# Kernel optimization log

Hardware: AMD Instinct MI355X
Metric: run time of the kernel (lower is better)

Reference implementation:

```python
import jax, jax.numpy as jnp
import numpy as np

B, D, F, T = 8192, 128, 128, 64


def setup_inputs() -> dict:
    key = jax.random.key(0)
    k1, k2, k3, k4 = jax.random.split(key, 4)
    inputs = jax.random.normal(k1, (B, D), dtype=jnp.float32)
    task_idx = jax.random.randint(k2, (B,), 0, T, dtype=jnp.int32)
    # default_kernel_init: normal * 1/sqrt(shape[1]) where shape=(T, D, F)
    kernels = jax.random.normal(k3, (T, D, F), dtype=jnp.float32) / jnp.sqrt(float(D))
    biases = jnp.zeros((T, F), dtype=jnp.float32)
    return {"inputs": inputs, "task_idx": task_idx, "kernels": kernels, "biases": biases}


def reference(inputs, task_idx, kernels, biases):
    # MoEDense forward (vector task_idx branch):
    #   y[b] = inputs[b] @ kernels[task_idx[b]] + biases[task_idx[b]]
    t = jnp.clip(task_idx, 0, kernels.shape[0] - 1)
    k_g = jnp.take(kernels, t, axis=0)          # [B, D, F] per-sample expert gather
    y = jnp.einsum('bd,bdf->bf', inputs, k_g)   # per-sample vec-mat
    y = y + jnp.take(biases, t, axis=0)
    return y
```

## Files before the change

### kernel.cpp

```cpp
#include <hip/hip_runtime.h>
#include <hip/hip_bf16.h>
#include <stdint.h>


#define D_ 128
#define F_ 128
#define T_ 64
#define TILE_M 64
#define TPE 3
#define LDA 136

typedef __attribute__((ext_vector_type(8))) short short8;
typedef __attribute__((ext_vector_type(4))) float floatx4;

__device__ __forceinline__ int clamp_t(int t) {
    return t < 0 ? 0 : (t > T_ - 1 ? T_ - 1 : t);
}

union frag_u {
    short8 s;
    __hip_bfloat162 p[4];
};

__global__ __launch_bounds__(256) void moe_fused(
    const float* __restrict__ x,
    const int*   __restrict__ tidx,
    const float* __restrict__ kern,
    const float* __restrict__ bias,
    float*       __restrict__ out)
{
    const int e    = blockIdx.x & 63;
    const int tb   = blockIdx.x >> 6;
    const int m0   = tb * TILE_M;
    const int tid  = threadIdx.x;
    const int wv   = tid >> 6;
    const int lane = tid & 63;
    const int quad = lane >> 4;
    const int l16  = lane & 15;
    const int n0w  = wv * 32;

    __shared__ int wtot[4];
    __shared__ int slot[TILE_M];
    __shared__ __align__(16) unsigned short A[TILE_M * LDA];

    const int4* tp = reinterpret_cast<const int4*>(tidx);
    int4 v[8];
    #pragma unroll
    for (int c = 0; c < 8; ++c) v[c] = tp[c * 256 + tid];

    int my = 0;
    #pragma unroll
    for (int c = 0; c < 8; ++c) {
        my += (clamp_t(v[c].x) == e);
        my += (clamp_t(v[c].y) == e);
        my += (clamp_t(v[c].z) == e);
        my += (clamp_t(v[c].w) == e);
    }
    int pre = my;
    #pragma unroll
    for (int d = 1; d < 64; d <<= 1) {
        int u = __shfl_up(pre, d);
        if (lane >= d) pre += u;
    }
    if (lane == 63) wtot[wv] = pre;
    __syncthreads();
    int wbase = 0, cnt = 0;
    #pragma unroll
    for (int w = 0; w < 4; ++w) {
        const int t = wtot[w];
        if (w < wv) wbase += t;
        cnt += t;
    }
    if (m0 >= cnt) return;
    const int base = wbase + pre - my;

    const float* Bp = kern + e * (D_ * F_);
    float c0r[4][8], c1r[4][8];
    #pragma unroll
    for (int kc = 0; kc < 4; ++kc) {
        const float* bp = Bp + (kc * 32 + quad * 8) * F_ + n0w + l16;
        #pragma unroll
        for (int j = 0; j < 8; ++j) {
            c0r[kc][j] = bp[j * F_];
            c1r[kc][j] = bp[j * F_ + 16];
        }
    }
    const float bs0 = bias[e * F_ + n0w + l16];
    const float bs1 = bias[e * F_ + n0w + l16 + 16];

    if (base < m0 + TILE_M && base + my > m0) {
        int run = base;
        #pragma unroll
        for (int c = 0; c < 8; ++c) {
            const int row4 = (c * 256 + tid) * 4;
            const int tt[4] = { v[c].x, v[c].y, v[c].z, v[c].w };
            #pragma unroll
            for (int j = 0; j < 4; ++j) {
                if (clamp_t(tt[j]) == e) {
                    if (run >= m0 && run < m0 + TILE_M)
                        slot[run - m0] = row4 + j;
                    ++run;
                }
            }
        }
    }
    __syncthreads();

    {
        const int row = tid >> 2;
        const int c   = (tid & 3) * 32;
        const int r   = (m0 + row < cnt) ? slot[row] : -1;
        float4 v0 = {0.f,0.f,0.f,0.f}, v1 = v0, v2 = v0, v3 = v0;
        float4 v4 = v0, v5 = v0, v6 = v0, v7 = v0;
        if (r >= 0) {
            const float4* xp = reinterpret_cast<const float4*>(x + r * D_ + c);
            v0 = xp[0]; v1 = xp[1]; v2 = xp[2]; v3 = xp[3];
            v4 = xp[4]; v5 = xp[5]; v6 = xp[6]; v7 = xp[7];
        }
        frag_u h0, h1, h2, h3;
        h0.p[0] = __float22bfloat162_rn({v0.x, v0.y});
        h0.p[1] = __float22bfloat162_rn({v0.z, v0.w});
        h0.p[2] = __float22bfloat162_rn({v1.x, v1.y});
        h0.p[3] = __float22bfloat162_rn({v1.z, v1.w});
        h1.p[0] = __float22bfloat162_rn({v2.x, v2.y});
        h1.p[1] = __float22bfloat162_rn({v2.z, v2.w});
        h1.p[2] = __float22bfloat162_rn({v3.x, v3.y});
        h1.p[3] = __float22bfloat162_rn({v3.z, v3.w});
        h2.p[0] = __float22bfloat162_rn({v4.x, v4.y});
        h2.p[1] = __float22bfloat162_rn({v4.z, v4.w});
        h2.p[2] = __float22bfloat162_rn({v5.x, v5.y});
        h2.p[3] = __float22bfloat162_rn({v5.z, v5.w});
        h3.p[0] = __float22bfloat162_rn({v6.x, v6.y});
        h3.p[1] = __float22bfloat162_rn({v6.z, v6.w});
        h3.p[2] = __float22bfloat162_rn({v7.x, v7.y});
        h3.p[3] = __float22bfloat162_rn({v7.z, v7.w});
        *reinterpret_cast<short8*>(&A[row * LDA + c])      = h0.s;
        *reinterpret_cast<short8*>(&A[row * LDA + c + 8])  = h1.s;
        *reinterpret_cast<short8*>(&A[row * LDA + c + 16]) = h2.s;
        *reinterpret_cast<short8*>(&A[row * LDA + c + 24]) = h3.s;
    }
    __syncthreads();

    floatx4 acc0[4], acc1[4];
    #pragma unroll
    for (int m = 0; m < 4; ++m) {
        acc0[m] = (floatx4){0.f,0.f,0.f,0.f};
        acc1[m] = (floatx4){0.f,0.f,0.f,0.f};
    }

    #pragma unroll
    for (int kc = 0; kc < 4; ++kc) {
        const int k0 = kc * 32;
        frag_u b0, b1;
        #pragma unroll
        for (int j = 0; j < 4; ++j) {
            b0.p[j] = __float22bfloat162_rn({c0r[kc][2 * j], c0r[kc][2 * j + 1]});
            b1.p[j] = __float22bfloat162_rn({c1r[kc][2 * j], c1r[kc][2 * j + 1]});
        }
        #pragma unroll
        for (int m = 0; m < 4; ++m) {
            const short8 a = *reinterpret_cast<const short8*>(
                &A[(m * 16 + l16) * LDA + k0 + quad * 8]);
            acc0[m] = __builtin_amdgcn_mfma_f32_16x16x32_bf16(a, b0.s, acc0[m], 0, 0, 0);
            acc1[m] = __builtin_amdgcn_mfma_f32_16x16x32_bf16(a, b1.s, acc1[m], 0, 0, 0);
        }
    }

    #pragma unroll
    for (int m = 0; m < 4; ++m) {
        #pragma unroll
        for (int reg = 0; reg < 4; ++reg) {
            const int mr = m * 16 + quad * 4 + reg;
            if (m0 + mr < cnt) {
                const int r = slot[mr];
                out[r * F_ + n0w + l16]      = acc0[m][reg] + bs0;
                out[r * F_ + n0w + l16 + 16] = acc1[m][reg] + bs1;
            }
        }
    }
}

extern "C" void kernel_launch(void* const* d_in, const int* in_sizes, int n_in,
                              void* d_out, int out_size, void* d_ws, size_t ws_size,
                              hipStream_t stream) {
    const float* x    = (const float*)d_in[0];
    const int*   tidx = (const int*)d_in[1];
    const float* kern = (const float*)d_in[2];
    const float* bias = (const float*)d_in[3];
    float* out = (float*)d_out;
    (void)d_ws; (void)ws_size; (void)in_sizes; (void)n_in; (void)out_size;

    moe_fused<<<TPE * T_, 256, 0, stream>>>(x, tidx, kern, bias, out);
}
```

Baseline: 69.41 us.

## Split expert row binning into separate atomic-based kernel before MFMA pass

Replaces the per-block redundant scan of all 8192 task indices (each of 192 blocks re-reading and prefix-summing the full index array) with a separate binning kernel that uses global atomics to build per-expert row lists in workspace. The main kernel then just reads its expert's count and row slice. This removes redundant scanning work but adds a memset and an extra kernel launch, and row order within an expert becomes nondeterministic.

```diff
diff --git a/kernel.cpp b/kernel.cpp
--- a/kernel.cpp
+++ b/kernel.cpp
@@ -8,6 +8,7 @@
 #define T_ 64
 #define TILE_M 64
 #define TPE 3
+#define CAP (TILE_M * TPE)
 #define LDA 136
 
 typedef __attribute__((ext_vector_type(8))) short short8;
@@ -22,11 +23,20 @@
     __hip_bfloat162 p[4];
 };
 
-__global__ __launch_bounds__(256) void moe_fused(
+__global__ __launch_bounds__(256) void bin_rows(
+    const int* __restrict__ tidx, int* __restrict__ ws)
+{
+    const int i = blockIdx.x * 256 + threadIdx.x;
+    const int t = clamp_t(tidx[i]);
+    const int pos = atomicAdd(ws + t, 1);
+    if (pos < CAP) ws[T_ + t * CAP + pos] = i;
+}
+
+__global__ __launch_bounds__(256) void moe_mfma(
     const float* __restrict__ x,
-    const int*   __restrict__ tidx,
     const float* __restrict__ kern,
     const float* __restrict__ bias,
+    const int*   __restrict__ ws,
     float*       __restrict__ out)
 {
     const int e    = blockIdx.x & 63;
@@ -39,40 +49,19 @@
     const int l16  = lane & 15;
     const int n0w  = wv * 32;
 
-    __shared__ int wtot[4];
+    int cnt = ws[e];
+    cnt = cnt > CAP ? CAP : cnt;
+    if (m0 >= cnt) return;
+
     __shared__ int slot[TILE_M];
     __shared__ __align__(16) unsigned short A[TILE_M * LDA];
 
-    const int4* tp = reinterpret_cast<const int4*>(tidx);
-    int4 v[8];
-    #pragma unroll
-    for (int c = 0; c < 8; ++c) v[c] = tp[c * 256 + tid];
+    const int* __restrict__ rl = ws + T_ + e * CAP + m0;
 
-    int my = 0;
-    #pragma unroll
-    for (int c = 0; c < 8; ++c) {
-        my += (clamp_t(v[c].x) == e);
-        my += (clamp_t(v[c].y) == e);
-        my += (clamp_t(v[c].z) == e);
-        my += (clamp_t(v[c].w) == e);
-    }
-    int pre = my;
-    #pragma unroll
-    for (int d = 1; d < 64; d <<= 1) {
-        int u = __shfl_up(pre, d);
-        if (lane >= d) pre += u;
-    }
-    if (lane == 63) wtot[wv] = pre;
-    __syncthreads();
-    int wbase = 0, cnt = 0;
-    #pragma unroll
-    for (int w = 0; w < 4; ++w) {
-        const int t = wtot[w];
-        if (w < wv) wbase += t;
-        cnt += t;
-    }
-    if (m0 >= cnt) return;
-    const int base = wbase + pre - my;
+    const int arow = tid >> 2;
+    const int r    = (m0 + arow < cnt) ? rl[arow] : -1;
+
+    if (tid < TILE_M) slot[tid] = (m0 + tid < cnt) ? rl[tid] : -1;
 
     const float* Bp = kern + e * (D_ * F_);
     float c0r[4][8], c1r[4][8];
@@ -88,28 +77,8 @@
     const float bs0 = bias[e * F_ + n0w + l16];
     const float bs1 = bias[e * F_ + n0w + l16 + 16];
 
-    if (base < m0 + TILE_M && base + my > m0) {
-        int run = base;
-        #pragma unroll
-        for (int c = 0; c < 8; ++c) {
-            const int row4 = (c * 256 + tid) * 4;
-            const int tt[4] = { v[c].x, v[c].y, v[c].z, v[c].w };
-            #pragma unroll
-            for (int j = 0; j < 4; ++j) {
-                if (clamp_t(tt[j]) == e) {
-                    if (run >= m0 && run < m0 + TILE_M)
-                        slot[run - m0] = row4 + j;
-                    ++run;
-                }
-            }
-        }
-    }
-    __syncthreads();
-
     {
-        const int row = tid >> 2;
-        const int c   = (tid & 3) * 32;
-        const int r   = (m0 + row < cnt) ? slot[row] : -1;
+        const int c = (tid & 3) * 32;
         float4 v0 = {0.f,0.f,0.f,0.f}, v1 = v0, v2 = v0, v3 = v0;
         float4 v4 = v0, v5 = v0, v6 = v0, v7 = v0;
         if (r >= 0) {
@@ -134,10 +103,10 @@
         h3.p[1] = __float22bfloat162_rn({v6.z, v6.w});
         h3.p[2] = __float22bfloat162_rn({v7.x, v7.y});
         h3.p[3] = __float22bfloat162_rn({v7.z, v7.w});
-        *reinterpret_cast<short8*>(&A[row * LDA + c])      = h0.s;
-        *reinterpret_cast<short8*>(&A[row * LDA + c + 8])  = h1.s;
-        *reinterpret_cast<short8*>(&A[row * LDA + c + 16]) = h2.s;
-        *reinterpret_cast<short8*>(&A[row * LDA + c + 24]) = h3.s;
+        *reinterpret_cast<short8*>(&A[arow * LDA + c])      = h0.s;
+        *reinterpret_cast<short8*>(&A[arow * LDA + c + 8])  = h1.s;
+        *reinterpret_cast<short8*>(&A[arow * LDA + c + 16]) = h2.s;
+        *reinterpret_cast<short8*>(&A[arow * LDA + c + 24]) = h3.s;
     }
     __syncthreads();
 
@@ -172,9 +141,9 @@
         for (int reg = 0; reg < 4; ++reg) {
             const int mr = m * 16 + quad * 4 + reg;
             if (m0 + mr < cnt) {
-                const int r = slot[mr];
-                out[r * F_ + n0w + l16]      = acc0[m][reg] + bs0;
-                out[r * F_ + n0w + l16 + 16] = acc1[m][reg] + bs1;
+                const int rr = slot[mr];
+                out[rr * F_ + n0w + l16]      = acc0[m][reg] + bs0;
+                out[rr * F_ + n0w + l16 + 16] = acc1[m][reg] + bs1;
             }
         }
     }
@@ -188,7 +157,10 @@
     const float* kern = (const float*)d_in[2];
     const float* bias = (const float*)d_in[3];
     float* out = (float*)d_out;
-    (void)d_ws; (void)ws_size; (void)in_sizes; (void)n_in; (void)out_size;
+    int* ws = (int*)d_ws;
+    (void)ws_size; (void)in_sizes; (void)n_in; (void)out_size;
 
-    moe_fused<<<TPE * T_, 256, 0, stream>>>(x, tidx, kern, bias, out);
+    hipMemsetAsync(ws, 0, T_ * sizeof(int), stream);
+    bin_rows<<<8192 / 256, 256, 0, stream>>>(tidx, ws);
+    moe_mfma<<<TPE * T_, 256, 0, stream>>>(x, kern, bias, ws, out);
 }
```

Result: slower. 83.67 us (+20.5%).
